# Optimization experiments

Hardware: AMD Instinct MI355X
Metric: run time of the kernel (lower is better)

The kernel has to match this reference:

```python
import jax, jax.numpy as jnp
import numpy as np

EPS = 1e-3  # keras LayerNormalization default epsilon

def layer_norm(x, gamma, beta):
    mu = jnp.mean(x, axis=-1, keepdims=True)
    var = jnp.var(x, axis=-1, keepdims=True)
    return (x - mu) * jax.lax.rsqrt(var + EPS) * gamma + beta

def setup_inputs() -> dict:
    key = jax.random.key(0)
    ks = jax.random.split(key, 10)
    B, N, FD, AD, PD, DP = 4, 512, 256, 256, 128, 64
    s = lambda k, *sh: jax.random.normal(k, sh, dtype=jnp.float32)
    return {
        "F": s(ks[0], B, N, FD),
        "D": s(ks[1], B, N, N, DP),
        "Wq": s(ks[2], FD, AD) / np.sqrt(FD),
        "Wk": s(ks[3], FD, AD) / np.sqrt(FD),
        "Wv": s(ks[4], FD, AD) / np.sqrt(FD),
        "g_f": jnp.ones((FD,), jnp.float32),
        "b_f": jnp.zeros((FD,), jnp.float32),
        "g_p": jnp.ones((DP,), jnp.float32),
        "b_p": jnp.zeros((DP,), jnp.float32),
        "W_pt": s(ks[5], DP, PD) / np.sqrt(DP),
        "b_pt": jnp.zeros((PD,), jnp.float32),
        "W_ph": s(ks[6], PD, 1) / np.sqrt(PD),
    }

def reference(F, D, Wq, Wk, Wv, g_f, b_f, g_p, b_p, W_pt, b_pt, W_ph):
    # features path
    Fn = layer_norm(F, g_f, b_f)                       # [B,N,FD]
    Q = Fn @ Wq                                        # [B,N,AD]
    K = Fn @ Wk
    V = Fn @ Wv
    # pair-bias path: LN -> Dense(pairs_dim)+bias -> Dense(num_heads=1)
    Bn = layer_norm(D, g_p, b_p)                       # [B,N,N,DP]
    Bt = Bn @ W_pt + b_pt                              # [B,N,N,PD]
    bias = (Bt @ W_ph)[..., 0]                         # [B,N,N]
    scalar = 1.0 / jnp.sqrt(jnp.float32(Q.shape[-1]))
    A = jnp.einsum('bqd,bkd->bqk', Q, K) + bias        # QK^T + pair bias
    A = jax.nn.softmax(scalar * A, axis=-1)
    O = jnp.einsum('bqk,bkd->bqd', A, V)               # [B,N,AD]
    return jnp.sum(O, axis=-1)                         # [B,N]
```

## Files before the change

kernel.cpp:

```cpp
#include <hip/hip_runtime.h>
#include <cstddef>
#include <cstdint>

#define OFF_GW    0
#define OFF_WV    64
#define OFF_SC    320
#define OFF_VSUM  384
#define OFF_Q     2432
#define OFF_KT    526720

typedef float v4f __attribute__((ext_vector_type(4)));
typedef float v2f __attribute__((ext_vector_type(2)));

__global__ __launch_bounds__(256) void k0_consts(
    const float* __restrict__ Wv, const float* __restrict__ g_p,
    const float* __restrict__ b_p, const float* __restrict__ W_pt,
    const float* __restrict__ b_pt, const float* __restrict__ W_ph,
    float* __restrict__ ws) {
  int t = threadIdx.x;
  if (blockIdx.x < 64) {
    int row = blockIdx.x * 4 + (t >> 6);
    int l = t & 63;
    float s = 0.f;
#pragma unroll
    for (int j = 0; j < 4; ++j) s += Wv[row * 256 + l + 64 * j];
    for (int m = 32; m >= 1; m >>= 1) s += __shfl_xor(s, m);
    if (l == 0) ws[OFF_WV + row] = s;
  } else {
    __shared__ float wc_s[64];
    __shared__ float wph_s[128];
    if (t < 128) wph_s[t] = W_ph[t];
    __syncthreads();
    int c = t >> 2, sub = t & 3;
    float wc = 0.f;
#pragma unroll
    for (int j = 0; j < 32; ++j)
      wc += W_pt[c * 128 + sub * 32 + j] * wph_s[sub * 32 + j];
    wc += __shfl_xor(wc, 1);
    wc += __shfl_xor(wc, 2);
    if (sub == 0) {
      wc_s[c] = wc;
      ws[OFF_GW + c] = g_p[c] * wc;
    }
    __syncthreads();
    if (t == 0) {
      float sg = 0.f, bc = 0.f;
      for (int cc = 0; cc < 64; ++cc) {
        sg += g_p[cc] * wc_s[cc];
        bc += b_p[cc] * wc_s[cc];
      }
      for (int p = 0; p < 128; ++p) bc += b_pt[p] * wph_s[p];
      ws[OFF_SC] = sg;
      ws[OFF_SC + 1] = bc;
    }
  }
}

__global__ __launch_bounds__(256) void k1_ln_qk(
    const float* __restrict__ F, const float* __restrict__ Wq,
    const float* __restrict__ Wk, const float* __restrict__ g_f,
    const float* __restrict__ b_f, float* __restrict__ ws) {
  __shared__ __align__(16) float fn[8][260];
  __shared__ float smu[8], srn[8];
  int t = threadIdx.x;
  int g = blockIdx.x >> 1, h = blockIdx.x & 1;
  int row0 = g * 8;
  const float* Fp = F + (size_t)row0 * 256;
#pragma unroll
  for (int k = 0; k < 8; ++k) fn[k][t] = Fp[k * 256 + t];
  __syncthreads();
  int r = t >> 5, l32 = t & 31;
  float s1 = 0.f, s2 = 0.f;
#pragma unroll
  for (int m = 0; m < 8; ++m) {
    float x = fn[r][l32 + 32 * m];
    s1 += x;
    s2 += x * x;
  }
  for (int m = 16; m >= 1; m >>= 1) {
    s1 += __shfl_xor(s1, m);
    s2 += __shfl_xor(s2, m);
  }
  if (l32 == 0) {
    float mu = s1 * (1.f / 256.f);
    float var = s2 * (1.f / 256.f) - mu * mu;
    smu[r] = mu;
    srn[r] = rsqrtf(var + 1e-3f);
  }
  __syncthreads();
  float gf = g_f[t], bf = b_f[t];
#pragma unroll
  for (int k = 0; k < 8; ++k)
    fn[k][t] = (fn[k][t] - smu[k]) * srn[k] * gf + bf;
  __syncthreads();
  if (h == 0) {
    const float* wv = ws + OFF_WV;
    float s = 0.f;
#pragma unroll
    for (int m = 0; m < 8; ++m) s += fn[r][l32 + 32 * m] * wv[l32 + 32 * m];
    for (int m = 16; m >= 1; m >>= 1) s += __shfl_xor(s, m);
    if (l32 == 0) ws[OFF_VSUM + row0 + r] = s;
  }
  int matsel = t >> 7;
  int col = h * 128 + (t & 127);
  const float* W = matsel ? Wk : Wq;
  float acc[8] = {0, 0, 0, 0, 0, 0, 0, 0};
#pragma unroll 2
  for (int f = 0; f < 256; f += 4) {
    float w0 = W[(f + 0) * 256 + col];
    float w1 = W[(f + 1) * 256 + col];
    float w2 = W[(f + 2) * 256 + col];
    float w3 = W[(f + 3) * 256 + col];
#pragma unroll
    for (int k = 0; k < 8; ++k) {
      v4f x = *(const v4f*)(&fn[k][f]);
      acc[k] = fmaf(x.w, w3,
               fmaf(x.z, w2, fmaf(x.y, w1, fmaf(x.x, w0, acc[k]))));
    }
  }
  if (matsel == 0) {
    float* Out = ws + OFF_Q + (size_t)row0 * 256 + col;
#pragma unroll
    for (int k = 0; k < 8; ++k) Out[k * 256] = acc[k];
  } else {
    int bb = row0 >> 9, r0b = row0 & 511;
    float* Out = ws + OFF_KT + (size_t)bb * 131072 + (size_t)col * 512 + r0b;
    v4f o0 = {acc[0], acc[1], acc[2], acc[3]};
    v4f o1 = {acc[4], acc[5], acc[6], acc[7]};
    *(v4f*)Out = o0;
    *(v4f*)(Out + 4) = o1;
  }
}

__global__ __launch_bounds__(256) void kb_bias_attn(
    const float* __restrict__ D, const float* __restrict__ ws,
    float* __restrict__ out) {
  __shared__ float Sx[4][512];
  __shared__ __align__(16) float Qs[4][256];
  __shared__ float vs[512];
  int t = threadIdx.x;
  int w = t >> 6, l = t & 63;
  int b = blockIdx.x >> 7, tile = blockIdx.x & 127;
  int rowbase = b * 512 + tile * 4;

#pragma unroll
  for (int k = 0; k < 4; ++k)
    Qs[k][t] = ws[OFF_Q + (size_t)(rowbase + k) * 256 + t];
  vs[t] = ws[OFF_VSUM + b * 512 + t];
  vs[t + 256] = ws[OFF_VSUM + b * 512 + 256 + t];
  float sum_gw = ws[OFF_SC];
  float bconst = ws[OFF_SC + 1];
  v4f g[16];
#pragma unroll
  for (int p = 0; p < 16; ++p) g[p] = *(const v4f*)(ws + OFF_GW + p * 4);

  const float* Dw = D + (size_t)(rowbase + w) * (512 * 64);
#pragma unroll 1
  for (int i = 0; i < 8; ++i) {
    const v4f* e = (const v4f*)(Dw + (size_t)(i * 64 + l) * 64);
    v4f x[16];
#pragma unroll
    for (int p = 0; p < 16; ++p) x[p] = e[p];
    float s1 = 0.f, s2 = 0.f, sw = 0.f;
#pragma unroll
    for (int p = 0; p < 16; ++p) {
      v4f xx = x[p];
      s1 += xx.x + xx.y + xx.z + xx.w;
      s2 += xx.x * xx.x + xx.y * xx.y + xx.z * xx.z + xx.w * xx.w;
      sw += xx.x * g[p].x + xx.y * g[p].y + xx.z * g[p].z + xx.w * g[p].w;
    }
    float mu = s1 * (1.f / 64.f);
    float var = s2 * (1.f / 64.f) - mu * mu;
    float rn = rsqrtf(var + 1e-3f);
    Sx[w][i * 64 + l] = (rn * (sw - mu * sum_gw) + bconst) * 0.0625f;
  }
  __syncthreads();

  const float* Ktb = ws + OFF_KT + (size_t)b * 131072;
  float a0[4] = {0, 0, 0, 0}, a1[4] = {0, 0, 0, 0};
#pragma unroll 2
  for (int f4 = 0; f4 < 64; ++f4) {
    v4f qv0 = *(const v4f*)(&Qs[0][f4 * 4]);
    v4f qv1 = *(const v4f*)(&Qs[1][f4 * 4]);
    v4f qv2 = *(const v4f*)(&Qs[2][f4 * 4]);
    v4f qv3 = *(const v4f*)(&Qs[3][f4 * 4]);
#pragma unroll
    for (int ff = 0; ff < 4; ++ff) {
      v2f kv = *(const v2f*)(Ktb + (size_t)(f4 * 4 + ff) * 512 + 2 * t);
      a0[0] += qv0[ff] * kv.x; a1[0] += qv0[ff] * kv.y;
      a0[1] += qv1[ff] * kv.x; a1[1] += qv1[ff] * kv.y;
      a0[2] += qv2[ff] * kv.x; a1[2] += qv2[ff] * kv.y;
      a0[3] += qv3[ff] * kv.x; a1[3] += qv3[ff] * kv.y;
    }
  }
#pragma unroll
  for (int rr = 0; rr < 4; ++rr) {
    Sx[rr][2 * t]     += a0[rr] * 0.0625f;
    Sx[rr][2 * t + 1] += a1[rr] * 0.0625f;
  }
  __syncthreads();

  float m = -1e30f;
#pragma unroll
  for (int j = 0; j < 8; ++j) m = fmaxf(m, Sx[w][l + 64 * j]);
  for (int mm = 32; mm >= 1; mm >>= 1) m = fmaxf(m, __shfl_xor(m, mm));
  float se = 0.f, sv = 0.f;
#pragma unroll
  for (int j = 0; j < 8; ++j) {
    float ev = __expf(Sx[w][l + 64 * j] - m);
    se += ev;
    sv += ev * vs[l + 64 * j];
  }
  for (int mm = 32; mm >= 1; mm >>= 1) {
    se += __shfl_xor(se, mm);
    sv += __shfl_xor(sv, mm);
  }
  if (l == 0) out[rowbase + w] = sv / se;
}

extern "C" void kernel_launch(void* const* d_in, const int* in_sizes, int n_in,
                              void* d_out, int out_size, void* d_ws,
                              size_t ws_size, hipStream_t stream) {
  const float* F    = (const float*)d_in[0];
  const float* D    = (const float*)d_in[1];
  const float* Wq   = (const float*)d_in[2];
  const float* Wk   = (const float*)d_in[3];
  const float* Wv   = (const float*)d_in[4];
  const float* g_f  = (const float*)d_in[5];
  const float* b_f  = (const float*)d_in[6];
  const float* g_p  = (const float*)d_in[7];
  const float* b_p  = (const float*)d_in[8];
  const float* W_pt = (const float*)d_in[9];
  const float* b_pt = (const float*)d_in[10];
  const float* W_ph = (const float*)d_in[11];
  float* out = (float*)d_out;
  float* ws = (float*)d_ws;

  k0_consts<<<65, 256, 0, stream>>>(Wv, g_p, b_p, W_pt, b_pt, W_ph, ws);
  k1_ln_qk<<<512, 256, 0, stream>>>(F, Wq, Wk, g_f, b_f, ws);
  kb_bias_attn<<<512, 256, 0, stream>>>(D, ws, out);
}
```

Baseline: 428.4 us.

## Split pair-bias LayerNorm reduction into separate wide kernel before attention

Moves the streaming reduction over the 256MB pair tensor D out of the attention kernel into a dedicated kernel with 4096 blocks, one edge per thread. The bias is written to workspace and reloaded by the attention kernel. The aim is higher occupancy and more memory-level parallelism for the bandwidth-bound D read, which was limited to 512 blocks with a serial per-wave loop. The cost is an extra 4MB write and read of the bias plus one more kernel launch.

```diff
diff --git a/kernel.cpp b/kernel.cpp
--- a/kernel.cpp
+++ b/kernel.cpp
@@ -8,6 +8,7 @@
 #define OFF_VSUM  384
 #define OFF_Q     2432
 #define OFF_KT    526720
+#define OFF_BIAS  1051008
 
 typedef float v4f __attribute__((ext_vector_type(4)));
 typedef float v2f __attribute__((ext_vector_type(2)));
@@ -132,9 +133,37 @@
   }
 }
 
-__global__ __launch_bounds__(256) void kb_bias_attn(
-    const float* __restrict__ D, const float* __restrict__ ws,
-    float* __restrict__ out) {
+__global__ __launch_bounds__(256, 4) void kb1_bias(
+    const float* __restrict__ D, float* __restrict__ ws) {
+  __shared__ __align__(16) float gws[64];
+  int t = threadIdx.x;
+  if (t < 64) gws[t] = ws[OFF_GW + t];
+  float sum_gw = ws[OFF_SC];
+  float bconst = ws[OFF_SC + 1];
+  __syncthreads();
+
+  int e = blockIdx.x * 256 + t;
+  const v4f* ep = (const v4f*)(D + (size_t)e * 64);
+  v4f x[16];
+#pragma unroll
+  for (int p = 0; p < 16; ++p) x[p] = ep[p];
+  float s1 = 0.f, s2 = 0.f, sw = 0.f;
+#pragma unroll
+  for (int p = 0; p < 16; ++p) {
+    v4f xx = x[p];
+    v4f gv = *(const v4f*)(&gws[p * 4]);
+    s1 += xx.x + xx.y + xx.z + xx.w;
+    s2 += xx.x * xx.x + xx.y * xx.y + xx.z * xx.z + xx.w * xx.w;
+    sw += xx.x * gv.x + xx.y * gv.y + xx.z * gv.z + xx.w * gv.w;
+  }
+  float mu = s1 * (1.f / 64.f);
+  float var = s2 * (1.f / 64.f) - mu * mu;
+  float rn = rsqrtf(var + 1e-3f);
+  ws[OFF_BIAS + e] = (rn * (sw - mu * sum_gw) + bconst) * 0.0625f;
+}
+
+__global__ __launch_bounds__(256) void kb2_attn(
+    const float* __restrict__ ws, float* __restrict__ out) {
   __shared__ float Sx[4][512];
   __shared__ __align__(16) float Qs[4][256];
   __shared__ float vs[512];
@@ -148,31 +177,11 @@
     Qs[k][t] = ws[OFF_Q + (size_t)(rowbase + k) * 256 + t];
   vs[t] = ws[OFF_VSUM + b * 512 + t];
   vs[t + 256] = ws[OFF_VSUM + b * 512 + 256 + t];
-  float sum_gw = ws[OFF_SC];
-  float bconst = ws[OFF_SC + 1];
-  v4f g[16];
-#pragma unroll
-  for (int p = 0; p < 16; ++p) g[p] = *(const v4f*)(ws + OFF_GW + p * 4);
-
-  const float* Dw = D + (size_t)(rowbase + w) * (512 * 64);
-#pragma unroll 1
-  for (int i = 0; i < 8; ++i) {
-    const v4f* e = (const v4f*)(Dw + (size_t)(i * 64 + l) * 64);
-    v4f x[16];
-#pragma unroll
-    for (int p = 0; p < 16; ++p) x[p] = e[p];
-    float s1 = 0.f, s2 = 0.f, sw = 0.f;
-#pragma unroll
-    for (int p = 0; p < 16; ++p) {
-      v4f xx = x[p];
-      s1 += xx.x + xx.y + xx.z + xx.w;
-      s2 += xx.x * xx.x + xx.y * xx.y + xx.z * xx.z + xx.w * xx.w;
-      sw += xx.x * g[p].x + xx.y * g[p].y + xx.z * g[p].z + xx.w * g[p].w;
-    }
-    float mu = s1 * (1.f / 64.f);
-    float var = s2 * (1.f / 64.f) - mu * mu;
-    float rn = rsqrtf(var + 1e-3f);
-    Sx[w][i * 64 + l] = (rn * (sw - mu * sum_gw) + bconst) * 0.0625f;
+  const float* bb = ws + OFF_BIAS + (size_t)rowbase * 512;
+#pragma unroll
+  for (int rr = 0; rr < 4; ++rr) {
+    Sx[rr][t] = bb[rr * 512 + t];
+    Sx[rr][t + 256] = bb[rr * 512 + 256 + t];
   }
   __syncthreads();
 
@@ -237,6 +246,7 @@
   float* ws = (float*)d_ws;
 
   k0_consts<<<65, 256, 0, stream>>>(Wv, g_p, b_p, W_pt, b_pt, W_ph, ws);
+  kb1_bias<<<4096, 256, 0, stream>>>(D, ws);
   k1_ln_qk<<<512, 256, 0, stream>>>(F, Wq, Wk, g_f, b_f, ws);
-  kb_bias_attn<<<512, 256, 0, stream>>>(D, ws, out);
-}
+  kb2_attn<<<512, 256, 0, stream>>>(ws, out);
+}
```

After: 431.4 us. Within noise of the previous version (+0.7%).
